# Optimization experiments

Hardware: AMD Instinct MI355X
Metric: run time of the kernel (lower is better)

The kernel has to match this reference:

```python
import jax, jax.numpy as jnp
import numpy as np

NEG_BIG = -9e15

def setup_inputs() -> dict:
    key = jax.random.key(0)
    k1, k2, k3, k4 = jax.random.split(key, 4)
    N, Fin, Fout = 8192, 256, 128
    x = jax.random.normal(k1, (N, Fin), dtype=jnp.float32)
    adj = jax.random.randint(k2, (N, N), 0, 2, dtype=jnp.int32)
    # xavier-uniform-like init
    limW = float(np.sqrt(6.0 / (Fin + Fout)))
    W = jax.random.uniform(k3, (Fin, Fout), minval=-limW, maxval=limW, dtype=jnp.float32)
    lima = float(np.sqrt(6.0 / (2 * Fout + 1)))
    a = jax.random.uniform(k4, (2 * Fout, 1), minval=-lima, maxval=lima, dtype=jnp.float32)
    return {"x": x, "adj": adj, "W": W, "a": a}

def reference(x, adj, W, a, alpha=0.2):
    # h: (N, Fout)
    h = x @ W
    Fout = W.shape[1]
    # Split a into source/target halves: e[i,j] = leakyrelu(h_i·a1 + h_j·a2)
    a1, a2 = a[:Fout, 0], a[Fout:, 0]
    s = h @ a1  # (N,) row (source) scores
    t = h @ a2  # (N,) col (target) scores
    e = jax.nn.leaky_relu(s[:, None] + t[None, :], negative_slope=alpha)  # (N, N)
    e = jnp.where(adj > 0, e, NEG_BIG)
    attention = jax.nn.softmax(e, axis=1)
    # dropout omitted (eval mode / training=False)
    return attention @ h
```

## Files before the change

### kernel.cpp

```cpp
#include <hip/hip_runtime.h>
#include <hip/hip_bf16.h>

typedef __attribute__((ext_vector_type(8))) short short8;
typedef __attribute__((ext_vector_type(4))) short short4v;
typedef __attribute__((ext_vector_type(4))) float f32x4;

#define NR 8192
#define LOG2E 1.4426950408889634f

__device__ __forceinline__ short f2bf(float f) {
  return __builtin_bit_cast(short, __float2bfloat16(f));
}

__global__ __launch_bounds__(256) void k_gemm_h(const float* __restrict__ x,
                                                const float* __restrict__ W,
                                                const float* __restrict__ a,
                                                short* __restrict__ HT2,
                                                float* __restrict__ sv,
                                                float* __restrict__ tv) {
  __shared__ short WT[128][136];
  const int tid = threadIdx.x;
  const int w = tid >> 6;
  const int L = tid & 63;
  const int lm = L & 15;
  const int q = L >> 4;
  const int i0 = blockIdx.x * 64;

  f32x4 acc[8];
#pragma unroll
  for (int nn = 0; nn < 8; ++nn) acc[nn] = (f32x4){0.f, 0.f, 0.f, 0.f};

  for (int kc = 0; kc < 256; kc += 128) {
    if (kc) __syncthreads();
#pragma unroll
    for (int p = 0; p < 16; ++p) {
      int idx = p * 256 + tid;
      int k = idx >> 5;
      int f4 = (idx & 31) * 4;
      float4 v = *(const float4*)&W[(kc + k) * 128 + f4];
      WT[f4 + 0][k] = f2bf(v.x);
      WT[f4 + 1][k] = f2bf(v.y);
      WT[f4 + 2][k] = f2bf(v.z);
      WT[f4 + 3][k] = f2bf(v.w);
    }
    __syncthreads();
#pragma unroll
    for (int ks = 0; ks < 4; ++ks) {
      int row = i0 + 16 * w + lm;
      const float* xp = &x[(size_t)row * 256 + kc + ks * 32 + q * 8];
      float4 xa = *(const float4*)xp;
      float4 xb = *(const float4*)(xp + 4);
      short8 af;
      af[0] = f2bf(xa.x); af[1] = f2bf(xa.y); af[2] = f2bf(xa.z); af[3] = f2bf(xa.w);
      af[4] = f2bf(xb.x); af[5] = f2bf(xb.y); af[6] = f2bf(xb.z); af[7] = f2bf(xb.w);
#pragma unroll
      for (int nn = 0; nn < 8; ++nn) {
        short8 bf = *(const short8*)&WT[nn * 16 + lm][ks * 32 + q * 8];
        acc[nn] = __builtin_amdgcn_mfma_f32_16x16x32_bf16(af, bf, acc[nn], 0, 0, 0);
      }
    }
  }

  const int ib = i0 + 16 * w + 4 * q;
  const int tbase = (ib >> 5) * 4096 + (ib & 31);
  float a1v[8], a2v[8];
#pragma unroll
  for (int nn = 0; nn < 8; ++nn) {
    a1v[nn] = a[nn * 16 + lm];
    a2v[nn] = a[128 + nn * 16 + lm];
  }
  float sr[4] = {0.f, 0.f, 0.f, 0.f};
  float tr[4] = {0.f, 0.f, 0.f, 0.f};
#pragma unroll
  for (int nn = 0; nn < 8; ++nn) {
    int f = nn * 16 + lm;
    short4v o;
    o[0] = f2bf(acc[nn][0]);
    o[1] = f2bf(acc[nn][1]);
    o[2] = f2bf(acc[nn][2]);
    o[3] = f2bf(acc[nn][3]);
    *(short4v*)&HT2[tbase + f * 32] = o;
#pragma unroll
    for (int r = 0; r < 4; ++r) {
      sr[r] += acc[nn][r] * a1v[nn];
      tr[r] += acc[nn][r] * a2v[nn];
    }
  }
#pragma unroll
  for (int d = 1; d < 16; d <<= 1) {
#pragma unroll
    for (int r = 0; r < 4; ++r) {
      sr[r] += __shfl_xor(sr[r], d);
      tr[r] += __shfl_xor(tr[r], d);
    }
  }
  if (lm == 0) {
#pragma unroll
    for (int r = 0; r < 4; ++r) {
      sv[ib + r] = sr[r] * LOG2E;
      tv[ib + r] = tr[r] * LOG2E;
    }
  }
}

__global__ __launch_bounds__(512, 4) void k_flash(const int* __restrict__ adj,
                                                  const short* __restrict__ HT2,
                                                  const float* __restrict__ sv,
                                                  const float* __restrict__ tv,
                                                  float* __restrict__ part,
                                                  float* __restrict__ lpart) {
  __shared__ short lds_s[32768];
  unsigned* ldsw = (unsigned*)lds_s;
  const int tid = threadIdx.x;
  const int w = tid >> 6;
  const int L = tid & 63;
  const int lm = L & 15;
  const int q = L >> 4;
  const int sp = blockIdx.x & 15;
  const int it = blockIdx.x >> 4;
  const int i0 = it * 128;

  const int row0 = i0 + 16 * w + lm;
  const float s0 = sv[row0];
  const size_t ar0 = (size_t)row0 * NR;

  f32x4 acc[8];
#pragma unroll
  for (int nn = 0; nn < 8; ++nn) acc[nn] = (f32x4){0.f, 0.f, 0.f, 0.f};
  float l0 = 0.f;

  const int tile0 = sp * 16;
  int jb = tile0 * 32 + q * 8;
  int4 sa00 = *(const int4*)&adj[ar0 + jb];
  int4 sa01 = *(const int4*)&adj[ar0 + jb + 4];

  for (int t = 0; t < 16; ++t) {
    if ((t & 7) == 0) {
      __syncthreads();
      const int pbase_t = tile0 + t;
#pragma unroll
      for (int z = 0; z < 8; ++z) {
        int id = z * 512 + tid;
        int tt = id >> 9;
        int k = id & 511;
        int f = k >> 2, c = k & 3;
        uint4 v = *(const uint4*)&HT2[(size_t)(pbase_t + tt) * 4096 + k * 8];
        int cs = c ^ ((f >> 1) & 3);
        *(uint4*)&ldsw[tt * 2048 + f * 16 + cs * 4] = v;
      }
      __syncthreads();
    }
    int4 a00 = sa00, a01 = sa01;
    if (t + 1 < 16) {
      int jn = (tile0 + t + 1) * 32 + q * 8;
      sa00 = *(const int4*)&adj[ar0 + jn];
      sa01 = *(const int4*)&adj[ar0 + jn + 4];
    }
    const int jc = (tile0 + t) * 32 + q * 8;
    float4 tv0 = *(const float4*)&tv[jc];
    float4 tv1 = *(const float4*)&tv[jc + 4];
    const int tt = t & 7;
    short8 bf[8];
#pragma unroll
    for (int nn = 0; nn < 8; ++nn) {
      int f = nn * 16 + lm;
      bf[nn] = *(const short8*)&ldsw[tt * 2048 + f * 16 + ((q ^ ((f >> 1) & 3)) * 4)];
    }

    int av0[8] = {a00.x, a00.y, a00.z, a00.w, a01.x, a01.y, a01.z, a01.w};
    float tvl[8] = {tv0.x, tv0.y, tv0.z, tv0.w, tv1.x, tv1.y, tv1.z, tv1.w};
    short8 p0;
#pragma unroll
    for (int e = 0; e < 8; ++e) {
      float v0 = s0 + tvl[e];
      float e0 = fmaxf(v0, 0.2f * v0);
      float pp0 = (av0[e] > 0) ? __builtin_amdgcn_exp2f(e0) : 0.f;
      l0 += pp0;
      p0[e] = f2bf(pp0);
    }
#pragma unroll
    for (int nn = 0; nn < 8; ++nn)
      acc[nn] = __builtin_amdgcn_mfma_f32_16x16x32_bf16(p0, bf[nn], acc[nn], 0, 0, 0);
  }
  __syncthreads();

  float* my = (float*)lds_s + w * 2048;
#pragma unroll
  for (int nn = 0; nn < 8; ++nn)
#pragma unroll
    for (int r = 0; r < 4; ++r)
      my[(4 * q + r) * 128 + nn * 16 + lm] = acc[nn][r];
  float* pbase = part + ((size_t)sp * NR + i0 + 16 * w) * 128;
#pragma unroll
  for (int c = 0; c < 8; ++c) {
    int idx = (c * 64 + L) * 4;
    *(float4*)&pbase[idx] = *(const float4*)&my[idx];
  }

  l0 += __shfl_xor(l0, 16);
  l0 += __shfl_xor(l0, 32);
  if (q == 0) lpart[sp * NR + row0] = l0;
}

__global__ __launch_bounds__(256) void k_reduce(const float* __restrict__ part,
                                                const float* __restrict__ lpart,
                                                float* __restrict__ out, int S) {
  int idx4 = blockIdx.x * 256 + threadIdx.x;
  int idx = idx4 * 4;
  int i = idx >> 7;
  float4 sum = {0.f, 0.f, 0.f, 0.f};
  for (int sp = 0; sp < S; ++sp) {
    float4 v = *(const float4*)&part[(size_t)sp * (NR * 128) + idx];
    sum.x += v.x; sum.y += v.y; sum.z += v.z; sum.w += v.w;
  }
  float l = 0.f;
  for (int sp = 0; sp < S; ++sp) l += lpart[sp * NR + i];
  float inv = (l > 0.f) ? 1.f / l : 0.f;
  float4 o = {sum.x * inv, sum.y * inv, sum.z * inv, sum.w * inv};
  *(float4*)&out[idx] = o;
}

extern "C" void kernel_launch(void* const* d_in, const int* in_sizes, int n_in,
                              void* d_out, int out_size, void* d_ws, size_t ws_size,
                              hipStream_t stream) {
  const float* x = (const float*)d_in[0];
  const int* adj = (const int*)d_in[1];
  const float* W = (const float*)d_in[2];
  const float* a = (const float*)d_in[3];
  float* out = (float*)d_out;

  char* ws = (char*)d_ws;
  short* HT2 = (short*)(ws + 0);
  float* sv = (float*)(ws + 2097152);
  float* tv = (float*)(ws + 2129920);
  float* lpart = (float*)(ws + 2162688);
  float* part = (float*)(ws + 2719744);

  const int S = 16;

  hipLaunchKernelGGL(k_gemm_h, dim3(128), dim3(256), 0, stream, x, W, a, HT2, sv, tv);
  hipLaunchKernelGGL(k_flash, dim3(64 * S), dim3(512), 0, stream, adj, HT2, sv, tv,
                     part, lpart);
  hipLaunchKernelGGL(k_reduce, dim3((NR * 128) / 1024), dim3(256), 0, stream, part,
                     lpart, out, S);
}
```

Baseline: 415.3 us.

## Split key dimension across waves in-block and fuse reduction into flash kernel

Each block now owns 16 rows, and its 8 waves each cover a different 1024-column slice of the key dimension. H tiles are read straight from global memory instead of being staged in LDS. The partial accumulators and row sums are reduced across waves in LDS and normalized in-kernel, which removes the partial-output buffers and the separate reduce kernel. The cost is that LDS sharing of H across the 8 waves is gone (each wave reads its own H slice), and the grid drops to 512 blocks, so occupancy and latency hiding may suffer.

Result: slower. 451.8 us (+8.8%).

```diff
diff --git a/kernel.cpp b/kernel.cpp
--- a/kernel.cpp
+++ b/kernel.cpp
@@ -107,117 +107,87 @@
                                                   const short* __restrict__ HT2,
                                                   const float* __restrict__ sv,
                                                   const float* __restrict__ tv,
-                                                  float* __restrict__ part,
-                                                  float* __restrict__ lpart) {
-  __shared__ short lds_s[32768];
-  unsigned* ldsw = (unsigned*)lds_s;
+                                                  float* __restrict__ out) {
+  __shared__ float red[8][16][128];
   const int tid = threadIdx.x;
   const int w = tid >> 6;
   const int L = tid & 63;
   const int lm = L & 15;
   const int q = L >> 4;
-  const int sp = blockIdx.x & 15;
-  const int it = blockIdx.x >> 4;
-  const int i0 = it * 128;
-
-  const int row0 = i0 + 16 * w + lm;
-  const float s0 = sv[row0];
-  const size_t ar0 = (size_t)row0 * NR;
+  const int i0 = blockIdx.x * 16;
+  const int row = i0 + lm;
+  const float s0 = sv[row];
+  const size_t ar = (size_t)row * NR;
 
   f32x4 acc[8];
 #pragma unroll
   for (int nn = 0; nn < 8; ++nn) acc[nn] = (f32x4){0.f, 0.f, 0.f, 0.f};
   float l0 = 0.f;
 
-  const int tile0 = sp * 16;
-  int jb = tile0 * 32 + q * 8;
-  int4 sa00 = *(const int4*)&adj[ar0 + jb];
-  int4 sa01 = *(const int4*)&adj[ar0 + jb + 4];
-
-  for (int t = 0; t < 16; ++t) {
-    if ((t & 7) == 0) {
-      __syncthreads();
-      const int pbase_t = tile0 + t;
-#pragma unroll
-      for (int z = 0; z < 8; ++z) {
-        int id = z * 512 + tid;
-        int tt = id >> 9;
-        int k = id & 511;
-        int f = k >> 2, c = k & 3;
-        uint4 v = *(const uint4*)&HT2[(size_t)(pbase_t + tt) * 4096 + k * 8];
-        int cs = c ^ ((f >> 1) & 3);
-        *(uint4*)&ldsw[tt * 2048 + f * 16 + cs * 4] = v;
-      }
-      __syncthreads();
-    }
-    int4 a00 = sa00, a01 = sa01;
-    if (t + 1 < 16) {
-      int jn = (tile0 + t + 1) * 32 + q * 8;
-      sa00 = *(const int4*)&adj[ar0 + jn];
-      sa01 = *(const int4*)&adj[ar0 + jn + 4];
-    }
-    const int jc = (tile0 + t) * 32 + q * 8;
-    float4 tv0 = *(const float4*)&tv[jc];
-    float4 tv1 = *(const float4*)&tv[jc + 4];
-    const int tt = t & 7;
+  const int t0 = w * 32;
+  int jb = t0 * 32 + q * 8;
+  int4 sa0 = *(const int4*)&adj[ar + jb];
+  int4 sa1 = *(const int4*)&adj[ar + jb + 4];
+
+  for (int t = t0; t < t0 + 32; ++t) {
+    int4 a0 = sa0, a1 = sa1;
+    if (t + 1 < t0 + 32) {
+      int jn = (t + 1) * 32 + q * 8;
+      sa0 = *(const int4*)&adj[ar + jn];
+      sa1 = *(const int4*)&adj[ar + jn + 4];
+    }
+    const int jc = t * 32 + q * 8;
+    float4 tva = *(const float4*)&tv[jc];
+    float4 tvb = *(const float4*)&tv[jc + 4];
+    const short* hp = &HT2[(size_t)t * 4096 + lm * 32 + q * 8];
     short8 bf[8];
 #pragma unroll
-    for (int nn = 0; nn < 8; ++nn) {
-      int f = nn * 16 + lm;
-      bf[nn] = *(const short8*)&ldsw[tt * 2048 + f * 16 + ((q ^ ((f >> 1) & 3)) * 4)];
-    }
-
-    int av0[8] = {a00.x, a00.y, a00.z, a00.w, a01.x, a01.y, a01.z, a01.w};
-    float tvl[8] = {tv0.x, tv0.y, tv0.z, tv0.w, tv1.x, tv1.y, tv1.z, tv1.w};
+    for (int nn = 0; nn < 8; ++nn) bf[nn] = *(const short8*)&hp[nn * 512];
+
+    int av[8] = {a0.x, a0.y, a0.z, a0.w, a1.x, a1.y, a1.z, a1.w};
+    float tvl[8] = {tva.x, tva.y, tva.z, tva.w, tvb.x, tvb.y, tvb.z, tvb.w};
     short8 p0;
 #pragma unroll
     for (int e = 0; e < 8; ++e) {
       float v0 = s0 + tvl[e];
       float e0 = fmaxf(v0, 0.2f * v0);
-      float pp0 = (av0[e] > 0) ? __builtin_amdgcn_exp2f(e0) : 0.f;
-      l0 += pp0;
-      p0[e] = f2bf(pp0);
+      float pp = (av[e] > 0) ? __builtin_amdgcn_exp2f(e0) : 0.f;
+      l0 += pp;
+      p0[e] = f2bf(pp);
     }
 #pragma unroll
     for (int nn = 0; nn < 8; ++nn)
       acc[nn] = __builtin_amdgcn_mfma_f32_16x16x32_bf16(p0, bf[nn], acc[nn], 0, 0, 0);
   }
-  __syncthreads();
-
-  float* my = (float*)lds_s + w * 2048;
-#pragma unroll
-  for (int nn = 0; nn < 8; ++nn)
-#pragma unroll
-    for (int r = 0; r < 4; ++r)
-      my[(4 * q + r) * 128 + nn * 16 + lm] = acc[nn][r];
-  float* pbase = part + ((size_t)sp * NR + i0 + 16 * w) * 128;
-#pragma unroll
-  for (int c = 0; c < 8; ++c) {
-    int idx = (c * 64 + L) * 4;
-    *(float4*)&pbase[idx] = *(const float4*)&my[idx];
-  }
-
+
+  float* scratch = &red[0][0][0];
   l0 += __shfl_xor(l0, 16);
   l0 += __shfl_xor(l0, 32);
-  if (q == 0) lpart[sp * NR + row0] = l0;
-}
-
-__global__ __launch_bounds__(256) void k_reduce(const float* __restrict__ part,
-                                                const float* __restrict__ lpart,
-                                                float* __restrict__ out, int S) {
-  int idx4 = blockIdx.x * 256 + threadIdx.x;
-  int idx = idx4 * 4;
-  int i = idx >> 7;
-  float4 sum = {0.f, 0.f, 0.f, 0.f};
-  for (int sp = 0; sp < S; ++sp) {
-    float4 v = *(const float4*)&part[(size_t)sp * (NR * 128) + idx];
-    sum.x += v.x; sum.y += v.y; sum.z += v.z; sum.w += v.w;
-  }
-  float l = 0.f;
-  for (int sp = 0; sp < S; ++sp) l += lpart[sp * NR + i];
-  float inv = (l > 0.f) ? 1.f / l : 0.f;
-  float4 o = {sum.x * inv, sum.y * inv, sum.z * inv, sum.w * inv};
-  *(float4*)&out[idx] = o;
+  if (L < 16) scratch[w * 16 + lm] = l0;
+  __syncthreads();
+  const int idx = tid * 4;
+  const int r_ = idx >> 7;
+  const int f_ = idx & 127;
+  float lsum = 0.f;
+#pragma unroll
+  for (int ww = 0; ww < 8; ++ww) lsum += scratch[ww * 16 + r_];
+  __syncthreads();
+#pragma unroll
+  for (int nn = 0; nn < 8; ++nn)
+#pragma unroll
+    for (int r = 0; r < 4; ++r)
+      red[w][4 * q + r][nn * 16 + lm] = acc[nn][r];
+  __syncthreads();
+  f32x4 sum = (f32x4){0.f, 0.f, 0.f, 0.f};
+#pragma unroll
+  for (int ww = 0; ww < 8; ++ww) {
+    const f32x4 v = *(const f32x4*)&red[ww][r_][f_];
+    sum[0] += v[0]; sum[1] += v[1]; sum[2] += v[2]; sum[3] += v[3];
+  }
+  float inv = (lsum > 0.f) ? 1.f / lsum : 0.f;
+  f32x4 o;
+  o[0] = sum[0] * inv; o[1] = sum[1] * inv; o[2] = sum[2] * inv; o[3] = sum[3] * inv;
+  *(f32x4*)&out[(size_t)(i0 + r_) * 128 + f_] = o;
 }
 
 extern "C" void kernel_launch(void* const* d_in, const int* in_sizes, int n_in,
@@ -233,14 +203,7 @@
   short* HT2 = (short*)(ws + 0);
   float* sv = (float*)(ws + 2097152);
   float* tv = (float*)(ws + 2129920);
-  float* lpart = (float*)(ws + 2162688);
-  float* part = (float*)(ws + 2719744);
-
-  const int S = 16;
 
   hipLaunchKernelGGL(k_gemm_h, dim3(128), dim3(256), 0, stream, x, W, a, HT2, sv, tv);
-  hipLaunchKernelGGL(k_flash, dim3(64 * S), dim3(512), 0, stream, adj, HT2, sv, tv,
-                     part, lpart);
-  hipLaunchKernelGGL(k_reduce, dim3((NR * 128) / 1024), dim3(256), 0, stream, part,
-                     lpart, out, S);
-}
+  hipLaunchKernelGGL(k_flash, dim3(512), dim3(512), 0, stream, adj, HT2, sv, tv, out);
+}
```
